# Kernel tuning notes

Measured on AMD Instinct MI355X. Metric: run time of the kernel, lower is better.

## Reference

```python
import jax, jax.numpy as jnp
import numpy as np

E = 16          # total experts (two halves of 8)
E_HALF = 8
K = 2           # top-k per token
CAP_FACTOR = 2  # expert capacity factor over the average load


def setup_inputs() -> dict:
    key = jax.random.key(0)
    ks = jax.random.split(key, 6)
    N, D, F = 16384, 1024, 1024  # tokens, d_model, d_ff (repo uses d_ff == d_model)
    s = 0.02
    return {
        "moe_inp": jax.random.normal(ks[0], (N, D), jnp.float32),
        "gate_w": jax.random.normal(ks[1], (D, E), jnp.float32) * s,   # gate Linear(d_model, 16)
        "gate_b": jnp.zeros((E,), jnp.float32),
        "route_w": jax.random.normal(ks[2], (D, 1), jnp.float32) * s,  # self.weights Linear(d_model, 1)
        "route_b": jnp.zeros((1,), jnp.float32),
        "W1": jax.random.normal(ks[3], (E, D, F), jnp.float32) * s,    # htoh4 per expert
        "b1": jnp.zeros((E, F), jnp.float32),
        "W2": jax.random.normal(ks[4], (E, F, D), jnp.float32) * s,    # h4toh per expert
        "b2": jnp.zeros((E, D), jnp.float32),
    }


def reference(moe_inp, gate_w, gate_b, route_w, route_b, W1, b1, W2, b2):
    N, D = moe_inp.shape
    # --- gate: logits over 16 experts; half 1 -> experts [0,8), half 2 -> experts [8,16)
    logits = moe_inp @ gate_w + gate_b                       # [N, E]
    val1, idx1 = jax.lax.top_k(logits[:, :E_HALF], K)        # [N, K]
    score1 = jax.nn.softmax(val1, axis=-1)
    val2, idx2 = jax.lax.top_k(logits[:, E_HALF:], K)
    score2 = jax.nn.softmax(val2, axis=-1)
    idx2 = idx2 + E_HALF                                     # shift into second expert range (gate_top_k_idx_2 + 8)
    # --- hard binary split of tokens via sigmoid(Linear(d,1)) > 0.5
    group1 = jax.nn.sigmoid(moe_inp @ route_w + route_b) > 0.5   # [N, 1]
    idx = jnp.where(group1, idx1, idx2)                      # [N, K] combined routing
    score = jnp.where(group1, score1, score2)                # [N, K]
    # --- dispatch: flatten (token, slot) pairs, capacity-bucket per expert
    T = N * K
    C = CAP_FACTOR * T // E                                  # expert capacity
    flat_idx = idx.reshape(-1)                               # [T]
    flat_x = jnp.repeat(moe_inp, K, axis=0)                  # [T, D]
    onehot = jax.nn.one_hot(flat_idx, E, dtype=jnp.int32)    # [T, E]
    pos_in_e = (jnp.cumsum(onehot, axis=0) * onehot).sum(axis=1) - 1  # [T] slot within expert
    valid = pos_in_e < C
    safe_pos = jnp.where(valid, pos_in_e, 0)
    buf = jnp.zeros((E, C, D), moe_inp.dtype).at[flat_idx, safe_pos].add(
        jnp.where(valid[:, None], flat_x, 0.0))              # [E, C, D] contiguous per-expert inputs
    # --- grouped expert FFN: relu(x W1 + b1) W2 + b2 (dropout = identity in eval)
    h = jax.nn.relu(jnp.einsum('ecd,edf->ecf', buf, W1) + b1[:, None, :])
    y = jnp.einsum('ecf,efd->ecd', h, W2) + b2[:, None, :]   # [E, C, D]
    # --- gather back and combine with gate scores
    y_flat = jnp.where(valid[:, None], y[flat_idx, safe_pos], 0.0)   # [T, D]
    out = (y_flat.reshape(N, K, D) * score[..., None]).sum(axis=1)   # [N, D]
    return out
```

## Files before the change

kernel.cpp:

```cpp
#include <hip/hip_runtime.h>
#include <hip/hip_bf16.h>
#include <stdint.h>

#define N_TOK 16384
#define DMODEL 1024
#define EXP 16
#define CAP 4096
#define TT 32768

typedef __bf16 bf16x8 __attribute__((ext_vector_type(8)));
typedef __bf16 bf16x4 __attribute__((ext_vector_type(4)));
typedef float  f32x4  __attribute__((ext_vector_type(4)));

__device__ __forceinline__ void gl_lds16(const void* g, void* s) {
  __builtin_amdgcn_global_load_lds(
      (__attribute__((address_space(1))) void*)(void*)g,
      (__attribute__((address_space(3))) void*)s, 16, 0, 0);
}

__device__ __forceinline__ float bfbits2f(unsigned short u) {
  return __uint_as_float(((unsigned)u) << 16);
}

#define FENCE asm volatile("" ::: "memory")
#define BAR() do { FENCE; __builtin_amdgcn_s_barrier(); FENCE; } while (0)

__global__ __launch_bounds__(256) void prep_kernel(const float* __restrict__ W1,
                                                   const float* __restrict__ W2,
                                                   __bf16* __restrict__ W1bt,
                                                   __bf16* __restrict__ W2bt,
                                                   const float* __restrict__ x,
                                                   const float* __restrict__ gw,
                                                   const float* __restrict__ gb,
                                                   const float* __restrict__ rw,
                                                   const float* __restrict__ rb,
                                                   int* __restrict__ idxo,
                                                   float* __restrict__ sco,
                                                   __bf16* __restrict__ Xb) {
  __shared__ char smem[21504];
  int bid = blockIdx.x;
  int tid = threadIdx.x;
  if (bid % 9 != 8) {
    int cb = bid - (bid + 1) / 9;
    float (*tile)[65] = (float(*)[65])smem;
    int tx = cb & 15;
    int ty = (cb >> 4) & 15;
    int e  = (cb >> 8) & 15;
    int which = (cb >> 12) & 1;
    const float* src = (which ? W2 : W1) + (size_t)e * DMODEL * DMODEL;
    __bf16*      dst = (which ? W2bt : W1bt) + (size_t)e * DMODEL * DMODEL;
    int r = tid >> 2;
    int cs = (tid & 3) * 16;
    int r0 = ty * 64, c0 = tx * 64;
    #pragma unroll
    for (int i = 0; i < 16; i += 4) {
      float4 v = *(const float4*)(src + (size_t)(r0 + r) * DMODEL + c0 + cs + i);
      tile[r][cs + i + 0] = v.x; tile[r][cs + i + 1] = v.y;
      tile[r][cs + i + 2] = v.z; tile[r][cs + i + 3] = v.w;
    }
    __syncthreads();
    bf16x8 o1, o2;
    #pragma unroll
    for (int i = 0; i < 8; i++) o1[i] = (__bf16)tile[cs + i][r];
    #pragma unroll
    for (int i = 0; i < 8; i++) o2[i] = (__bf16)tile[cs + 8 + i][r];
    {
      int n  = c0 + r;
      int g  = n >> 4, fr = n & 15;
      int k1 = r0 + cs;
      int c1 = k1 >> 5, fg1 = (k1 >> 3) & 3;
      int k2 = k1 + 8;
      int c2 = k2 >> 5, fg2 = (k2 >> 3) & 3;
      *(bf16x8*)(dst + ((size_t)(g * 32 + c1) * 512 + (fg1 * 16 + fr) * 8)) = o1;
      *(bf16x8*)(dst + ((size_t)(g * 32 + c2) * 512 + (fg2 * 16 + fr) * 8)) = o2;
    }
  } else {
    float* gws = (float*)smem;
    float* rws = (float*)(smem + 20480);
    int g = bid / 9;
    int w = tid >> 6, lane = tid & 63;
    int n0t = g * 16 + w * 4;
    const float* xr0 = x + (size_t)(n0t + 0) * DMODEL;
    const float* xr1 = x + (size_t)(n0t + 1) * DMODEL;
    const float* xr2 = x + (size_t)(n0t + 2) * DMODEL;
    const float* xr3 = x + (size_t)(n0t + 3) * DMODEL;

    float acc0[17], acc1[17], acc2[17], acc3[17];
    #pragma unroll
    for (int j = 0; j < 17; j++) { acc0[j] = 0.f; acc1[j] = 0.f; acc2[j] = 0.f; acc3[j] = 0.f; }

    for (int c = 0; c < 4; c++) {
      int c0 = c * 256;
      __syncthreads();
      #pragma unroll
      for (int q = tid, it = 0; it < 4; q += 256, it++) {
        float4 v = *(const float4*)(gw + c0 * 16 + q * 4);
        *(float4*)(gws + (q >> 2) * 20 + (q & 3) * 4) = v;
      }
      rws[tid] = rw[c0 + tid];
      __syncthreads();

      #pragma unroll
      for (int dv = 0; dv < 4; dv++) {
        int dl = dv * 64 + lane;
        int d  = c0 + dl;
        float x0 = xr0[d], x1 = xr1[d], x2 = xr2[d], x3 = xr3[d];
        Xb[(size_t)(n0t + 0) * DMODEL + d] = (__bf16)x0;
        Xb[(size_t)(n0t + 1) * DMODEL + d] = (__bf16)x1;
        Xb[(size_t)(n0t + 2) * DMODEL + d] = (__bf16)x2;
        Xb[(size_t)(n0t + 3) * DMODEL + d] = (__bf16)x3;
        const float* gp = gws + dl * 20;
        float4 g0 = *(const float4*)(gp);
        float4 g1 = *(const float4*)(gp + 4);
        float4 g2 = *(const float4*)(gp + 8);
        float4 g3 = *(const float4*)(gp + 12);
        float rv = rws[dl];
        float gj[16] = {g0.x, g0.y, g0.z, g0.w, g1.x, g1.y, g1.z, g1.w,
                        g2.x, g2.y, g2.z, g2.w, g3.x, g3.y, g3.z, g3.w};
        #pragma unroll
        for (int j = 0; j < 16; j++) {
          acc0[j] += x0 * gj[j]; acc1[j] += x1 * gj[j];
          acc2[j] += x2 * gj[j]; acc3[j] += x3 * gj[j];
        }
        acc0[16] += x0 * rv; acc1[16] += x1 * rv;
        acc2[16] += x2 * rv; acc3[16] += x3 * rv;
      }
    }

    #pragma unroll
    for (int o = 1; o < 64; o <<= 1) {
      #pragma unroll
      for (int j = 0; j < 17; j++) {
        acc0[j] += __shfl_xor(acc0[j], o);
        acc1[j] += __shfl_xor(acc1[j], o);
        acc2[j] += __shfl_xor(acc2[j], o);
        acc3[j] += __shfl_xor(acc3[j], o);
      }
    }
    if (lane == 0) {
      float* accs[4] = {acc0, acc1, acc2, acc3};
      #pragma unroll
      for (int tk = 0; tk < 4; tk++) {
        float* acc = accs[tk];
        int n = n0t + tk;
        float rv = acc[16] + rb[0];
        bool g1f = rv > 0.f;
        float c[8];
        #pragma unroll
        for (int j = 0; j < 8; j++)
          c[j] = (g1f ? acc[j] + gb[j] : acc[8 + j] + gb[8 + j]);
        int i1 = 0; float v1 = c[0];
        #pragma unroll
        for (int j = 1; j < 8; j++) { if (c[j] > v1) { v1 = c[j]; i1 = j; } }
        int i2 = -1; float v2 = -3.4e38f;
        #pragma unroll
        for (int j = 0; j < 8; j++) { if (j != i1 && c[j] > v2) { v2 = c[j]; i2 = j; } }
        float e2 = expf(v2 - v1);
        float den = 1.f + e2;
        int base = g1f ? 0 : 8;
        idxo[2 * n] = base + i1; idxo[2 * n + 1] = base + i2;
        sco[2 * n] = 1.f / den;  sco[2 * n + 1] = e2 / den;
      }
    }
  }
}

__global__ __launch_bounds__(1024) void scan_kernel(const int* __restrict__ idx,
                                                    float* __restrict__ sco,
                                                    int* __restrict__ rowlist,
                                                    int* __restrict__ cnt,
                                                    int* __restrict__ off) {
  __shared__ int hist[16 * 1024];
  int tid = threadIdx.x;
  #pragma unroll
  for (int e = 0; e < 16; e++) hist[e * 1024 + tid] = 0;
  __syncthreads();
  int base = tid * 32;
  for (int i = 0; i < 32; i++) {
    int e = idx[base + i];
    hist[e * 1024 + tid]++;
  }
  __syncthreads();
  int w = tid >> 6, lane = tid & 63;
  {
    int e = w;
    int running = 0;
    for (int cch = 0; cch < 16; cch++) {
      int v = hist[e * 1024 + cch * 64 + lane];
      int orig = v;
      #pragma unroll
      for (int o = 1; o < 64; o <<= 1) {
        int nv = __shfl_up(v, o);
        if (lane >= o) v += nv;
      }
      hist[e * 1024 + cch * 64 + lane] = running + v - orig;
      running += __shfl(v, 63);
    }
    if (lane == 0) cnt[e] = running;
  }
  __syncthreads();
  if (tid == 0) {
    int o = 0;
    for (int e = 0; e < 16; e++) {
      int c = cnt[e]; if (c > CAP) c = CAP;
      off[e] = o; cnt[e] = c; o += c;
    }
  }
  __syncthreads();
  for (int i = 0; i < 32; i++) {
    int t = base + i;
    int e = idx[t];
    int r = hist[e * 1024 + tid]++;
    if (r < CAP) rowlist[e * CAP + r] = t;
    else sco[t] = 0.f;
  }
}

#define GBM 128
#define GBN 128
#define GBK 64
#define NKT (DMODEL / GBK)

__global__ __launch_bounds__(256, 2) void moe_gemm(const __bf16* __restrict__ A,
                                                   const __bf16* __restrict__ Bf,
                                                   const float* __restrict__ bias,
                                                   __bf16* __restrict__ out,
                                                   const int* __restrict__ rowlist,
                                                   const int* __restrict__ cnt,
                                                   const int* __restrict__ off,
                                                   int mode) {
  __shared__ char lds[32768];
  int bx = blockIdx.x;
  int em = (bx & 7) * 64 + (bx >> 3);
  int e  = em >> 5;
  int m0 = (em & 31) * GBM;
  int ce = cnt[e];
  if (m0 >= ce) return;
  int n0 = blockIdx.y * GBN;
  int oe = off[e];
  int tid = threadIdx.x;

  const __bf16* aP[4];
  #pragma unroll
  for (int j = 0; j < 4; j++) {
    int c = j * 256 + tid;
    int srow = c >> 3;
    int gsrc = (c & 7) ^ (srow & 7);
    int rr = m0 + srow; if (rr > ce - 1) rr = ce - 1;
    size_t arow;
    if (mode == 0) arow = (size_t)(rowlist[e * CAP + rr] >> 1);
    else           arow = (size_t)(oe + rr);
    aP[j] = A + arow * DMODEL + gsrc * 8;
  }

  int w = tid >> 6, lane = tid & 63;
  int wr = (w >> 1) * 64;
  int wc = (w & 1) * 64;
  int fr = lane & 15, fg = lane >> 4;

  int aRd = wr * 128 + fr * 128;
  int gk0 = ((fg)     ^ (fr & 7)) * 16;
  int gk1 = ((4 | fg) ^ (fr & 7)) * 16;

  const __bf16* bF = Bf + (size_t)e * DMODEL * DMODEL
                        + (size_t)(((n0 + wc) >> 4) * 32) * 512
                        + (size_t)lane * 8;

  f32x4 acc[4][4];
  #pragma unroll
  for (int mi = 0; mi < 4; mi++)
    #pragma unroll
    for (int ni = 0; ni < 4; ni++)
      #pragma unroll
      for (int l = 0; l < 4; l++) acc[mi][ni][l] = 0.f;

  auto stA = [&](int s) {
    char* dst = lds + (s & 1) * 16384;
    #pragma unroll
    for (int j = 0; j < 4; j++)
      gl_lds16(aP[j] + s * 64, dst + (size_t)(j * 256 + tid) * 16);
  };

  bf16x8 bqA[4][2], bqB[4][2];

  auto ldB = [&](int s, bf16x8 (&dst)[4][2]) {
    #pragma unroll
    for (int ni = 0; ni < 4; ni++) {
      dst[ni][0] = *(const bf16x8*)(bF + ni * 16384 + (2 * s) * 512);
      dst[ni][1] = *(const bf16x8*)(bF + ni * 16384 + (2 * s + 1) * 512);
    }
  };

  ldB(0, bqA);
  FENCE;
  stA(0); stA(1);
  asm volatile("s_waitcnt vmcnt(4)" ::: "memory");
  BAR();

  bf16x8 afA[4][2];

  auto giter = [&](int T, bf16x8 (&cur)[4][2], bf16x8 (&nxt)[4][2]) {
    const char* Ab = lds + (T & 1) * 16384 + aRd;
    #pragma unroll
    for (int mi = 0; mi < 4; mi++) {
      afA[mi][0] = *(const bf16x8*)(Ab + mi * 2048 + gk0);
      afA[mi][1] = *(const bf16x8*)(Ab + mi * 2048 + gk1);
    }
    if (T + 1 < NKT) ldB(T + 1, nxt);
    asm volatile("s_waitcnt lgkmcnt(0)" ::: "memory");
    __builtin_amdgcn_sched_barrier(0);
    __builtin_amdgcn_s_setprio(1);
    #pragma unroll
    for (int kk = 0; kk < 2; kk++)
      #pragma unroll
      for (int mi = 0; mi < 4; mi++) {
        acc[mi][0] = __builtin_amdgcn_mfma_f32_16x16x32_bf16(afA[mi][kk], cur[0][kk], acc[mi][0], 0, 0, 0);
        acc[mi][1] = __builtin_amdgcn_mfma_f32_16x16x32_bf16(afA[mi][kk], cur[1][kk], acc[mi][1], 0, 0, 0);
      }
    __builtin_amdgcn_s_setprio(0);
    BAR();
    if (T <= NKT - 3) stA(T + 2);
    __builtin_amdgcn_s_setprio(1);
    #pragma unroll
    for (int kk = 0; kk < 2; kk++)
      #pragma unroll
      for (int mi = 0; mi < 4; mi++) {
        acc[mi][2] = __builtin_amdgcn_mfma_f32_16x16x32_bf16(afA[mi][kk], cur[2][kk], acc[mi][2], 0, 0, 0);
        acc[mi][3] = __builtin_amdgcn_mfma_f32_16x16x32_bf16(afA[mi][kk], cur[3][kk], acc[mi][3], 0, 0, 0);
      }
    __builtin_amdgcn_s_setprio(0);
    if (T <= NKT - 3)      asm volatile("s_waitcnt vmcnt(12)" ::: "memory");
    else if (T == NKT - 2) asm volatile("s_waitcnt vmcnt(8)" ::: "memory");
    BAR();
  };

  for (int tt = 0; tt < NKT; tt += 2) {
    giter(tt, bqA, bqB);
    giter(tt + 1, bqB, bqA);
  }

  float bcol[4];
  #pragma unroll
  for (int ni = 0; ni < 4; ni++)
    bcol[ni] = bias[(size_t)e * DMODEL + n0 + wc + ni * 16 + fr];
  #pragma unroll
  for (int mi = 0; mi < 4; mi++) {
    #pragma unroll
    for (int r = 0; r < 4; r++) {
      int grow = m0 + wr + mi * 16 + fg * 4 + r;
      if (grow >= ce) continue;
      size_t orow = (mode == 0) ? (size_t)(oe + grow)
                                : (size_t)rowlist[e * CAP + grow];
      __bf16* op = out + orow * DMODEL + n0 + wc + fr;
      #pragma unroll
      for (int ni = 0; ni < 4; ni++) {
        float v = acc[mi][ni][r] + bcol[ni];
        if (mode == 0) v = fmaxf(v, 0.f);
        op[ni * 16] = (__bf16)v;
      }
    }
  }
}

__global__ __launch_bounds__(256) void combine_kernel(const __bf16* __restrict__ y,
                                                      const float* __restrict__ sco,
                                                      float* __restrict__ out) {
  int n = blockIdx.x;
  int d = threadIdx.x * 4;
  float s0 = sco[2 * n], s1 = sco[2 * n + 1];
  ushort4 a = *(const ushort4*)((const unsigned short*)(y + (size_t)(2 * n) * DMODEL + d));
  ushort4 b = *(const ushort4*)((const unsigned short*)(y + (size_t)(2 * n + 1) * DMODEL + d));
  float4 o;
  o.x = s0 * bfbits2f(a.x) + s1 * bfbits2f(b.x);
  o.y = s0 * bfbits2f(a.y) + s1 * bfbits2f(b.y);
  o.z = s0 * bfbits2f(a.z) + s1 * bfbits2f(b.z);
  o.w = s0 * bfbits2f(a.w) + s1 * bfbits2f(b.w);
  *(float4*)(out + (size_t)n * DMODEL + d) = o;
}

extern "C" void kernel_launch(void* const* d_in, const int* in_sizes, int n_in,
                              void* d_out, int out_size, void* d_ws, size_t ws_size,
                              hipStream_t stream) {
  const float* moe = (const float*)d_in[0];
  const float* gw  = (const float*)d_in[1];
  const float* gb  = (const float*)d_in[2];
  const float* rw  = (const float*)d_in[3];
  const float* rb  = (const float*)d_in[4];
  const float* W1  = (const float*)d_in[5];
  const float* b1  = (const float*)d_in[6];
  const float* W2  = (const float*)d_in[7];
  const float* b2  = (const float*)d_in[8];
  float* out = (float*)d_out;

  char* p = (char*)d_ws;
  __bf16* Xb   = (__bf16*)p; p += (size_t)N_TOK * DMODEL * 2;
  __bf16* W1bt = (__bf16*)p; p += (size_t)EXP * DMODEL * DMODEL * 2;
  __bf16* W2bt = (__bf16*)p; p += (size_t)EXP * DMODEL * DMODEL * 2;
  __bf16* hbuf = (__bf16*)p; p += (size_t)TT * DMODEL * 2;
  __bf16* ybuf = (__bf16*)p; p += (size_t)TT * DMODEL * 2;
  int*   idxb   = (int*)p;   p += (size_t)TT * 4;
  float* scoreb = (float*)p; p += (size_t)TT * 4;
  int*   rowlist = (int*)p;  p += (size_t)EXP * CAP * 4;
  int*   cntb    = (int*)p;  p += 64;
  int*   offb    = (int*)p;  p += 64;

  prep_kernel<<<dim3(9216), dim3(256), 0, stream>>>(W1, W2, W1bt, W2bt,
                                                    moe, gw, gb, rw, rb,
                                                    idxb, scoreb, Xb);
  scan_kernel<<<dim3(1), dim3(1024), 0, stream>>>(idxb, scoreb, rowlist, cntb, offb);
  moe_gemm<<<dim3(512, 8), dim3(256), 0, stream>>>(Xb, W1bt, b1, hbuf, rowlist, cntb, offb, 0);
  moe_gemm<<<dim3(512, 8), dim3(256), 0, stream>>>(hbuf, W2bt, b2, ybuf, rowlist, cntb, offb, 1);
  combine_kernel<<<dim3(16384), dim3(256), 0, stream>>>(ybuf, scoreb, out);
}
```

Baseline: 388.1 us.

## Stage B tiles through LDS with halved K tile and higher occupancy

The expert GEMM now streams weight fragments into LDS with global_load_lds, alongside the activation tile, instead of loading them straight into registers. The K tile is halved to 32, which halves each LDS buffer to 8 KB, and the launch bound asks for 4 blocks per CU instead of 2. The aim is to cut register pressure and raise occupancy so memory latency is hidden better. In exchange there are twice as many barrier-separated iterations with fewer MFMAs each, and the A tile layout drops its XOR swizzle, which may cause LDS bank conflicts.

```diff
diff --git a/kernel.cpp b/kernel.cpp
--- a/kernel.cpp
+++ b/kernel.cpp
@@ -218,10 +218,10 @@
 
 #define GBM 128
 #define GBN 128
-#define GBK 64
+#define GBK 32
 #define NKT (DMODEL / GBK)
 
-__global__ __launch_bounds__(256, 2) void moe_gemm(const __bf16* __restrict__ A,
+__global__ __launch_bounds__(256, 4) void moe_gemm(const __bf16* __restrict__ A,
                                                    const __bf16* __restrict__ Bf,
                                                    const float* __restrict__ bias,
                                                    __bf16* __restrict__ out,
@@ -240,17 +240,27 @@
   int oe = off[e];
   int tid = threadIdx.x;
 
-  const __bf16* aP[4];
-  #pragma unroll
-  for (int j = 0; j < 4; j++) {
-    int c = j * 256 + tid;
-    int srow = c >> 3;
-    int gsrc = (c & 7) ^ (srow & 7);
+  const __bf16* aP[2];
+  #pragma unroll
+  for (int j = 0; j < 2; j++) {
+    int lin = j * 256 + tid;
+    int srow = lin >> 2;
+    int chunk = lin & 3;
     int rr = m0 + srow; if (rr > ce - 1) rr = ce - 1;
     size_t arow;
     if (mode == 0) arow = (size_t)(rowlist[e * CAP + rr] >> 1);
     else           arow = (size_t)(oe + rr);
-    aP[j] = A + arow * DMODEL + gsrc * 8;
+    aP[j] = A + arow * DMODEL + chunk * 8;
+  }
+  const __bf16* bP[2];
+  int g0 = n0 >> 4;
+  #pragma unroll
+  for (int j = 0; j < 2; j++) {
+    int lin = j * 256 + tid;
+    int grp = lin >> 6;
+    int ln  = lin & 63;
+    bP[j] = Bf + (size_t)e * DMODEL * DMODEL
+               + (size_t)((g0 + grp) * 32) * 512 + (size_t)ln * 8;
   }
 
   int w = tid >> 6, lane = tid & 63;
@@ -258,13 +268,8 @@
   int wc = (w & 1) * 64;
   int fr = lane & 15, fg = lane >> 4;
 
-  int aRd = wr * 128 + fr * 128;
-  int gk0 = ((fg)     ^ (fr & 7)) * 16;
-  int gk1 = ((4 | fg) ^ (fr & 7)) * 16;
-
-  const __bf16* bF = Bf + (size_t)e * DMODEL * DMODEL
-                        + (size_t)(((n0 + wc) >> 4) * 32) * 512
-                        + (size_t)lane * 8;
+  int aRd = wr * 64 + fr * 64 + fg * 16;
+  int bRd = 16384 + (w & 1) * 4096 + lane * 16;
 
   f32x4 acc[4][4];
   #pragma unroll
@@ -275,68 +280,51 @@
       for (int l = 0; l < 4; l++) acc[mi][ni][l] = 0.f;
 
   auto stA = [&](int s) {
-    char* dst = lds + (s & 1) * 16384;
-    #pragma unroll
-    for (int j = 0; j < 4; j++)
-      gl_lds16(aP[j] + s * 64, dst + (size_t)(j * 256 + tid) * 16);
+    char* dst = lds + (s & 1) * 8192;
+    gl_lds16(aP[0] + s * 32, dst + (size_t)tid * 16);
+    gl_lds16(aP[1] + s * 32, dst + (size_t)(256 + tid) * 16);
   };
-
-  bf16x8 bqA[4][2], bqB[4][2];
-
-  auto ldB = [&](int s, bf16x8 (&dst)[4][2]) {
-    #pragma unroll
-    for (int ni = 0; ni < 4; ni++) {
-      dst[ni][0] = *(const bf16x8*)(bF + ni * 16384 + (2 * s) * 512);
-      dst[ni][1] = *(const bf16x8*)(bF + ni * 16384 + (2 * s + 1) * 512);
-    }
+  auto stB = [&](int s) {
+    char* dst = lds + 16384 + (s & 1) * 8192;
+    gl_lds16(bP[0] + s * 512, dst + (size_t)tid * 16);
+    gl_lds16(bP[1] + s * 512, dst + (size_t)(256 + tid) * 16);
   };
 
-  ldB(0, bqA);
-  FENCE;
-  stA(0); stA(1);
+  stA(0); stB(0); stA(1); stB(1);
   asm volatile("s_waitcnt vmcnt(4)" ::: "memory");
   BAR();
 
-  bf16x8 afA[4][2];
-
-  auto giter = [&](int T, bf16x8 (&cur)[4][2], bf16x8 (&nxt)[4][2]) {
-    const char* Ab = lds + (T & 1) * 16384 + aRd;
-    #pragma unroll
-    for (int mi = 0; mi < 4; mi++) {
-      afA[mi][0] = *(const bf16x8*)(Ab + mi * 2048 + gk0);
-      afA[mi][1] = *(const bf16x8*)(Ab + mi * 2048 + gk1);
-    }
-    if (T + 1 < NKT) ldB(T + 1, nxt);
+  for (int t = 0; t < NKT; ++t) {
+    const char* Ab = lds + (t & 1) * 8192 + aRd;
+    const char* Bb = lds + (t & 1) * 8192 + bRd;
+
+    bf16x8 af[4], bq[4];
+    #pragma unroll
+    for (int mi = 0; mi < 4; mi++) af[mi] = *(const bf16x8*)(Ab + mi * 1024);
+    #pragma unroll
+    for (int ni = 0; ni < 4; ni++) bq[ni] = *(const bf16x8*)(Bb + ni * 1024);
     asm volatile("s_waitcnt lgkmcnt(0)" ::: "memory");
     __builtin_amdgcn_sched_barrier(0);
     __builtin_amdgcn_s_setprio(1);
     #pragma unroll
-    for (int kk = 0; kk < 2; kk++)
-      #pragma unroll
-      for (int mi = 0; mi < 4; mi++) {
-        acc[mi][0] = __builtin_amdgcn_mfma_f32_16x16x32_bf16(afA[mi][kk], cur[0][kk], acc[mi][0], 0, 0, 0);
-        acc[mi][1] = __builtin_amdgcn_mfma_f32_16x16x32_bf16(afA[mi][kk], cur[1][kk], acc[mi][1], 0, 0, 0);
-      }
+    for (int mi = 0; mi < 4; mi++) {
+      acc[mi][0] = __builtin_amdgcn_mfma_f32_16x16x32_bf16(af[mi], bq[0], acc[mi][0], 0, 0, 0);
+      acc[mi][1] = __builtin_amdgcn_mfma_f32_16x16x32_bf16(af[mi], bq[1], acc[mi][1], 0, 0, 0);
+    }
     __builtin_amdgcn_s_setprio(0);
     BAR();
-    if (T <= NKT - 3) stA(T + 2);
+
+    if (t <= NKT - 3) { stA(t + 2); stB(t + 2); }
     __builtin_amdgcn_s_setprio(1);
     #pragma unroll
-    for (int kk = 0; kk < 2; kk++)
-      #pragma unroll
-      for (int mi = 0; mi < 4; mi++) {
-        acc[mi][2] = __builtin_amdgcn_mfma_f32_16x16x32_bf16(afA[mi][kk], cur[2][kk], acc[mi][2], 0, 0, 0);
-        acc[mi][3] = __builtin_amdgcn_mfma_f32_16x16x32_bf16(afA[mi][kk], cur[3][kk], acc[mi][3], 0, 0, 0);
-      }
+    for (int mi = 0; mi < 4; mi++) {
+      acc[mi][2] = __builtin_amdgcn_mfma_f32_16x16x32_bf16(af[mi], bq[2], acc[mi][2], 0, 0, 0);
+      acc[mi][3] = __builtin_amdgcn_mfma_f32_16x16x32_bf16(af[mi], bq[3], acc[mi][3], 0, 0, 0);
+    }
     __builtin_amdgcn_s_setprio(0);
-    if (T <= NKT - 3)      asm volatile("s_waitcnt vmcnt(12)" ::: "memory");
-    else if (T == NKT - 2) asm volatile("s_waitcnt vmcnt(8)" ::: "memory");
+    if (t <= NKT - 3)      asm volatile("s_waitcnt vmcnt(4)" ::: "memory");
+    else if (t == NKT - 2) asm volatile("s_waitcnt vmcnt(0)" ::: "memory");
     BAR();
-  };
-
-  for (int tt = 0; tt < NKT; tt += 2) {
-    giter(tt, bqA, bqB);
-    giter(tt + 1, bqB, bqA);
   }
 
   float bcol[4];
```

New measurement: 345.2 us. 1.12x faster.
